# Performance work log

Hardware: AMD Instinct MI355X
Metric: run time of the kernel (lower is better)

Reference implementation:

```python
import jax, jax.numpy as jnp
import numpy as np

EPS = 1e-7  # K.epsilon()
ROUTINGS = 3

def squash(v):
    # v: [..., dim_capsule]
    s2 = jnp.sum(jnp.square(v), axis=-1, keepdims=True)
    scale = s2 / (1.0 + s2) / jnp.sqrt(s2 + EPS)
    return scale * v

def setup_inputs() -> dict:
    key = jax.random.key(0)
    k1, k2 = jax.random.split(key)
    B, IN_CAPS, IN_DIM = 256, 1152, 8
    NUM_CAPS, DIM_CAPS = 10, 16
    inputs = jax.random.normal(k1, (B, IN_CAPS, IN_DIM), dtype=jnp.float32)
    W = jax.random.normal(k2, (NUM_CAPS, IN_CAPS, DIM_CAPS, IN_DIM), dtype=jnp.float32) * 0.05
    return {"inputs": inputs, "W": W}

def reference(inputs, W):
    # inputs: [B, I, Q]; W: [J, I, P, Q]
    # inputs_hat[b,j,i,p] = sum_q W[j,i,p,q] * inputs[b,i,q]
    inputs_hat = jnp.einsum('jipq,biq->bjip', W, inputs)  # [B, J, I, P]
    B, J, I, P = inputs_hat.shape
    b = jnp.zeros((B, J, I), dtype=inputs_hat.dtype)
    outputs = None
    for r in range(ROUTINGS):
        c = jax.nn.softmax(b, axis=1)                      # over num_capsule J
        s = jnp.einsum('bji,bjip->bjp', c, inputs_hat)     # [B, J, P]
        outputs = squash(s)
        if r < ROUTINGS - 1:
            b = b + jnp.einsum('bjp,bjip->bji', outputs, inputs_hat)
    return outputs
```

## Files before the change

### kernel.cpp

```cpp
#include <hip/hip_runtime.h>

typedef _Float16 h2 __attribute__((ext_vector_type(2)));
typedef _Float16 h8 __attribute__((ext_vector_type(8)));
typedef float f4 __attribute__((ext_vector_type(4)));

#define BB 256
#define II 1152
#define QQ 8
#define JJ 10
#define PP 16

#define BT 16
#define IT 8
#define NBT (BB / BT)
#define NIT (II / IT)
#define XRH 72
#define WTILE (IT * PP * QQ)

#define NW (JJ * II * PP * QQ)
#define NX (BB * II * QQ)
#define NS (BB * JJ * PP)
#define LOG2E 1.4426950408889634f

template <int CTRL>
__device__ __forceinline__ float dpp_add(float v) {
    int s = __builtin_bit_cast(int, v);
    int t = __builtin_amdgcn_update_dpp(0, s, CTRL, 0xF, 0xF, true);
    return v + __builtin_bit_cast(float, t);
}
__device__ __forceinline__ float row_sum16(float v) {
    v = dpp_add<0xB1>(v);
    v = dpp_add<0x4E>(v);
    v = dpp_add<0x124>(v);
    v = dpp_add<0x128>(v);
    return v;
}
template <int CTRL>
__device__ __forceinline__ h2 dpp_add_pk(h2 v) {
    int s = __builtin_bit_cast(int, v);
    int t = __builtin_amdgcn_update_dpp(0, s, CTRL, 0xF, 0xF, true);
    return v + __builtin_bit_cast(h2, t);
}
__device__ __forceinline__ h2 row_sum16_pk(h2 v) {
    v = dpp_add_pk<0xB1>(v);
    v = dpp_add_pk<0x4E>(v);
    v = dpp_add_pk<0x124>(v);
    v = dpp_add_pk<0x128>(v);
    return v;
}

__device__ __forceinline__ float dot8(h8 w, h8 x) {
    h2 w0 = __builtin_shufflevector(w, w, 0, 1), w1 = __builtin_shufflevector(w, w, 2, 3);
    h2 w2 = __builtin_shufflevector(w, w, 4, 5), w3 = __builtin_shufflevector(w, w, 6, 7);
    h2 x0 = __builtin_shufflevector(x, x, 0, 1), x1 = __builtin_shufflevector(x, x, 2, 3);
    h2 x2 = __builtin_shufflevector(x, x, 4, 5), x3 = __builtin_shufflevector(x, x, 6, 7);
    float acc = __builtin_amdgcn_fdot2(w0, x0, 0.0f, false);
    acc = __builtin_amdgcn_fdot2(w1, x1, acc, false);
    acc = __builtin_amdgcn_fdot2(w2, x2, acc, false);
    acc = __builtin_amdgcn_fdot2(w3, x3, acc, false);
    return acc;
}

__global__ __launch_bounds__(256) void prep_kernel(
    const float* __restrict__ X, const float* __restrict__ W,
    _Float16* __restrict__ Xh, _Float16* __restrict__ Wh,
    float* __restrict__ S)
{
    const int g = blockIdx.x * 256 + threadIdx.x;
    const int stride = gridDim.x * 256;
    typedef _Float16 h4 __attribute__((ext_vector_type(4)));
    for (int k = g; k < NW / 4; k += stride) {
        const float4 f = ((const float4*)W)[k];
        h4 o = { (_Float16)f.x, (_Float16)f.y, (_Float16)f.z, (_Float16)f.w };
        ((h4*)Wh)[k] = o;
    }
    for (int k = g; k < NX / 4; k += stride) {
        const float4 f = ((const float4*)X)[k];
        h4 o = { (_Float16)f.x, (_Float16)f.y, (_Float16)f.z, (_Float16)f.w };
        ((h4*)Xh)[k] = o;
    }
    const float4 z = {0.f, 0.f, 0.f, 0.f};
    for (int k = g; k < 3 * NS / 4; k += stride) ((float4*)S)[k] = z;
}

__global__ __launch_bounds__(256) void s0_mfma_kernel(
    const _Float16* __restrict__ Xh, const _Float16* __restrict__ Wh,
    float* __restrict__ S0)
{
    const int wid  = blockIdx.x * 4 + (threadIdx.x >> 6);
    const int lane = threadIdx.x & 63;
    const int bt  = wid / 80;
    const int rem = wid % 80;
    const int j   = rem >> 3;
    const int kc  = rem & 7;
    const int b0  = bt * 16;
    const int m    = lane & 15;
    const int quad = lane >> 4;
    const int ib   = kc * 144;

    const _Float16* ax = Xh + ((size_t)(b0 + m) * II + ib + quad) * QQ;
    const _Float16* bw = Wh + (((size_t)j * II + ib + quad) * PP + m) * QQ;

    f4 acc = {0.f, 0.f, 0.f, 0.f};
    for (int t = 0; t < 36; ++t) {
        const h8 a = *(const h8*)ax;
        const h8 b = *(const h8*)bw;
        acc = __builtin_amdgcn_mfma_f32_16x16x32_f16(a, b, acc, 0, 0, 0);
        ax += 4 * QQ;
        bw += (size_t)4 * PP * QQ;
    }
#pragma unroll
    for (int r = 0; r < 4; ++r)
        atomicAdd(&S0[((size_t)(b0 + quad * 4 + r) * JJ + j) * PP + m], 0.1f * acc[r]);
}

template <int MODE>
__global__ __launch_bounds__(256) void vv_kernel(
    const float* __restrict__ S, float* __restrict__ V0raw,
    float* __restrict__ VV)
{
    const int idx = blockIdx.x * 256 + threadIdx.x;
    const float s = S[idx];
    const float n2 = row_sum16(s * s);
    const float sc = n2 * __builtin_amdgcn_rcpf(1.0f + n2)
                        * __builtin_amdgcn_rsqf(n2 + 1e-7f);
    const float v = s * sc;
    if (MODE == 0) {
        V0raw[idx] = v;
        VV[idx] = v * LOG2E;
    } else {
        VV[idx] = (v + V0raw[idx]) * LOG2E;
    }
}

__global__ __launch_bounds__(256, 4) void pass_kernel(
    const _Float16* __restrict__ Xh,
    const _Float16* __restrict__ Wh,
    const float* __restrict__ VV,
    float* __restrict__ Sout)
{
    __shared__ _Float16 ws[JJ * WTILE];
    __shared__ _Float16 xs[BT * XRH];

    const int bt = blockIdx.x & (NBT - 1);
    const int it = blockIdx.x >> 4;
    const int b0 = bt * BT;
    const int i0 = it * IT;
    const int tid = threadIdx.x;

    {
        const size_t jstride = (size_t)II * PP * QQ;
        const _Float16* wsrc = Wh + (size_t)i0 * PP * QQ;
#pragma unroll
        for (int k = 0; k < 5; ++k) {
            const int c = tid + k * 256;
            const int j = c >> 7;
            const int r = c & 127;
            *(h8*)(ws + j * WTILE + r * 8) = *(const h8*)(wsrc + j * jstride + r * 8);
        }
        if (tid < 128) {
            const int xb = tid >> 3;
            const int xr = tid & 7;
            *(h8*)(xs + xb * XRH + xr * 8) =
                *(const h8*)(Xh + ((size_t)(b0 + xb) * II + i0) * QQ + xr * 8);
        }
    }
    __syncthreads();

    const int b_l = tid >> 4;
    const int p   = tid & 15;
    const int b   = b0 + b_l;

    float vv[JJ];
#pragma unroll
    for (int j = 0; j < JJ; ++j)
        vv[j] = VV[((size_t)b * JJ + j) * PP + p];

    float sacc[JJ];
#pragma unroll
    for (int j = 0; j < JJ; ++j) sacc[j] = 0.0f;

    const _Float16* wb = ws + p * QQ;
    const _Float16* xb = xs + b_l * XRH;

#pragma unroll
    for (int i = 0; i < IT; ++i) {
        const h8 x8 = *(const h8*)(xb + i * QQ);

        float h[JJ];
#pragma unroll
        for (int j = 0; j < JJ; ++j)
            h[j] = dot8(*(const h8*)(wb + j * WTILE + i * PP * QQ), x8);

        float e[JJ];
#pragma unroll
        for (int jp = 0; jp < JJ; jp += 2) {
            const h2 pk = __builtin_bit_cast(h2,
                __builtin_amdgcn_cvt_pkrtz(vv[jp] * h[jp],
                                           vv[jp + 1] * h[jp + 1]));
            const h2 r = row_sum16_pk(pk);
            e[jp]     = __builtin_amdgcn_exp2f((float)r.x);
            e[jp + 1] = __builtin_amdgcn_exp2f((float)r.y);
        }
        float a0 = (e[0] + e[1]) + (e[2] + e[3]);
        float a1 = (e[4] + e[5]) + (e[6] + e[7]);
        const float sum = (a0 + a1) + (e[8] + e[9]);
        const float inv = __builtin_amdgcn_rcpf(sum);
#pragma unroll
        for (int j = 0; j < JJ; ++j) sacc[j] += (e[j] * inv) * h[j];
    }

#pragma unroll
    for (int j = 0; j < JJ; ++j)
        atomicAdd(&Sout[((size_t)b * JJ + j) * PP + p], sacc[j]);
}

__global__ __launch_bounds__(256) void squash_out_kernel(const float* __restrict__ S,
                                                         float* __restrict__ V)
{
    const int idx = blockIdx.x * blockDim.x + threadIdx.x;
    if (idx >= BB * JJ) return;
    const float4* sp = (const float4*)(S + idx * PP);
    float4 a = sp[0], b4 = sp[1], c4 = sp[2], d4 = sp[3];
    float s2 = a.x * a.x + a.y * a.y + a.z * a.z + a.w * a.w +
               b4.x * b4.x + b4.y * b4.y + b4.z * b4.z + b4.w * b4.w +
               c4.x * c4.x + c4.y * c4.y + c4.z * c4.z + c4.w * c4.w +
               d4.x * d4.x + d4.y * d4.y + d4.z * d4.z + d4.w * d4.w;
    const float scale = s2 / (1.0f + s2) / sqrtf(s2 + 1e-7f);
    a.x *= scale; a.y *= scale; a.z *= scale; a.w *= scale;
    b4.x *= scale; b4.y *= scale; b4.z *= scale; b4.w *= scale;
    c4.x *= scale; c4.y *= scale; c4.z *= scale; c4.w *= scale;
    d4.x *= scale; d4.y *= scale; d4.z *= scale; d4.w *= scale;
    float4* vp = (float4*)(V + idx * PP);
    vp[0] = a; vp[1] = b4; vp[2] = c4; vp[3] = d4;
}

extern "C" void kernel_launch(void* const* d_in, const int* in_sizes, int n_in,
                              void* d_out, int out_size, void* d_ws, size_t ws_size,
                              hipStream_t stream)
{
    const float* X = (const float*)d_in[0];
    const float* W = (const float*)d_in[1];
    float* out = (float*)d_out;

    _Float16* Xh = (_Float16*)d_ws;
    _Float16* Wh = Xh + NX;
    float* S0 = (float*)(Wh + NW);
    float* S1 = S0 + NS;
    float* S2 = S1 + NS;
    float* V0raw = S2 + NS;
    float* VV1   = V0raw + NS;
    float* VV2   = VV1 + NS;

    const int grid  = NBT * NIT;
    const int vgrid = NS / 256;

    prep_kernel<<<1024, 256, 0, stream>>>(X, W, Xh, Wh, S0);
    s0_mfma_kernel<<<320, 256, 0, stream>>>(Xh, Wh, S0);
    vv_kernel<0><<<vgrid, 256, 0, stream>>>(S0, V0raw, VV1);
    pass_kernel<<<grid, 256, 0, stream>>>(Xh, Wh, VV1, S1);
    vv_kernel<1><<<vgrid, 256, 0, stream>>>(S1, V0raw, VV2);
    pass_kernel<<<grid, 256, 0, stream>>>(Xh, Wh, VV2, S2);
    squash_out_kernel<<<10, 256, 0, stream>>>(S2, out);
}
```

Baseline: 132.0 us.

## Restructure routing pass kernel around MFMA for agreement and weighted sum

The routing pass drops per-thread fdot2 dot products and uses MFMA twice. One MFMA contracts v with W to get per-(b,i,q) projections, which are then scaled by x and reduced over q with DPP to form logits. A second MFMA multiplies c·x by W to accumulate s, with partial sums collected in shared memory before the global atomics. W is loaded into LDS in a transposed layout read via ds_read_b64_tr_b16, and VV is stored in fp16. This cuts VALU work in the hot kernel, at the cost of more LDS traffic, LDS atomics, a lower occupancy bound (3) and extra fp16 rounding.

```diff
diff --git a/kernel.cpp b/kernel.cpp
--- a/kernel.cpp
+++ b/kernel.cpp
@@ -1,6 +1,7 @@
 #include <hip/hip_runtime.h>
 
 typedef _Float16 h2 __attribute__((ext_vector_type(2)));
+typedef _Float16 h4 __attribute__((ext_vector_type(4)));
 typedef _Float16 h8 __attribute__((ext_vector_type(8)));
 typedef float f4 __attribute__((ext_vector_type(4)));
 
@@ -15,7 +16,6 @@
 #define NBT (BB / BT)
 #define NIT (II / IT)
 #define XRH 72
-#define WTILE (IT * PP * QQ)
 
 #define NW (JJ * II * PP * QQ)
 #define NX (BB * II * QQ)
@@ -41,24 +41,11 @@
     int t = __builtin_amdgcn_update_dpp(0, s, CTRL, 0xF, 0xF, true);
     return v + __builtin_bit_cast(h2, t);
 }
-__device__ __forceinline__ h2 row_sum16_pk(h2 v) {
+__device__ __forceinline__ h2 row_sum8_pk(h2 v) {
     v = dpp_add_pk<0xB1>(v);
     v = dpp_add_pk<0x4E>(v);
-    v = dpp_add_pk<0x124>(v);
-    v = dpp_add_pk<0x128>(v);
+    v = dpp_add_pk<0x141>(v);
     return v;
-}
-
-__device__ __forceinline__ float dot8(h8 w, h8 x) {
-    h2 w0 = __builtin_shufflevector(w, w, 0, 1), w1 = __builtin_shufflevector(w, w, 2, 3);
-    h2 w2 = __builtin_shufflevector(w, w, 4, 5), w3 = __builtin_shufflevector(w, w, 6, 7);
-    h2 x0 = __builtin_shufflevector(x, x, 0, 1), x1 = __builtin_shufflevector(x, x, 2, 3);
-    h2 x2 = __builtin_shufflevector(x, x, 4, 5), x3 = __builtin_shufflevector(x, x, 6, 7);
-    float acc = __builtin_amdgcn_fdot2(w0, x0, 0.0f, false);
-    acc = __builtin_amdgcn_fdot2(w1, x1, acc, false);
-    acc = __builtin_amdgcn_fdot2(w2, x2, acc, false);
-    acc = __builtin_amdgcn_fdot2(w3, x3, acc, false);
-    return acc;
 }
 
 __global__ __launch_bounds__(256) void prep_kernel(
@@ -68,7 +55,6 @@
 {
     const int g = blockIdx.x * 256 + threadIdx.x;
     const int stride = gridDim.x * 256;
-    typedef _Float16 h4 __attribute__((ext_vector_type(4)));
     for (int k = g; k < NW / 4; k += stride) {
         const float4 f = ((const float4*)W)[k];
         h4 o = { (_Float16)f.x, (_Float16)f.y, (_Float16)f.z, (_Float16)f.w };
@@ -117,7 +103,7 @@
 template <int MODE>
 __global__ __launch_bounds__(256) void vv_kernel(
     const float* __restrict__ S, float* __restrict__ V0raw,
-    float* __restrict__ VV)
+    _Float16* __restrict__ VVh)
 {
     const int idx = blockIdx.x * 256 + threadIdx.x;
     const float s = S[idx];
@@ -127,20 +113,25 @@
     const float v = s * sc;
     if (MODE == 0) {
         V0raw[idx] = v;
-        VV[idx] = v * LOG2E;
+        VVh[idx] = (_Float16)(v * LOG2E);
     } else {
-        VV[idx] = (v + V0raw[idx]) * LOG2E;
-    }
-}
-
-__global__ __launch_bounds__(256, 4) void pass_kernel(
+        VVh[idx] = (_Float16)((v + V0raw[idx]) * LOG2E);
+    }
+}
+
+__global__ __launch_bounds__(256, 3) void pass_kernel(
+    const float* __restrict__ X,
     const _Float16* __restrict__ Xh,
     const _Float16* __restrict__ Wh,
-    const float* __restrict__ VV,
+    const _Float16* __restrict__ VVh,
     float* __restrict__ Sout)
 {
-    __shared__ _Float16 ws[JJ * WTILE];
-    __shared__ _Float16 xs[BT * XRH];
+    __shared__ _Float16 wtr[JJ * 4 * 256];
+    __shared__ _Float16 xna[BT * XRH];
+    __shared__ float    xtr[64 * 20];
+    __shared__ _Float16 vvs[16 * 168];
+    __shared__ float    cs[4][JJ][2][16];
+    __shared__ float    sacc[JJ * 16 * 17];
 
     const int bt = blockIdx.x & (NBT - 1);
     const int it = blockIdx.x >> 4;
@@ -156,63 +147,131 @@
             const int c = tid + k * 256;
             const int j = c >> 7;
             const int r = c & 127;
-            *(h8*)(ws + j * WTILE + r * 8) = *(const h8*)(wsrc + j * jstride + r * 8);
+            const int i = r >> 4;
+            const int p = r & 15;
+            const h8 v = *(const h8*)(wsrc + j * jstride + (size_t)r * 8);
+            *(h8*)(wtr + (j * 4 + (i >> 1)) * 256 + p * 16 + (i & 1) * 8) = v;
         }
         if (tid < 128) {
             const int xb = tid >> 3;
             const int xr = tid & 7;
-            *(h8*)(xs + xb * XRH + xr * 8) =
+            *(h8*)(xna + xb * XRH + xr * 8) =
                 *(const h8*)(Xh + ((size_t)(b0 + xb) * II + i0) * QQ + xr * 8);
         }
+        {
+            const int qh = tid & 1;
+            const int i  = (tid >> 1) & 7;
+            const int b  = tid >> 4;
+            const float4 v = *(const float4*)(X + ((size_t)(b0 + b) * II + i0 + i) * QQ + qh * 4);
+            const int row = i * 8 + qh * 4;
+            xtr[(row + 0) * 20 + b] = v.x;
+            xtr[(row + 1) * 20 + b] = v.y;
+            xtr[(row + 2) * 20 + b] = v.z;
+            xtr[(row + 3) * 20 + b] = v.w;
+        }
+#pragma unroll
+        for (int k = 0; k < 5; ++k) {
+            const int c = tid + k * 256;
+            const int b = c / 80;
+            const int rem = c - b * 80;
+            *(unsigned*)(vvs + b * 168 + rem * 2) =
+                *(const unsigned*)(VVh + (size_t)(b0 + b) * JJ * PP + rem * 2);
+        }
+#pragma unroll
+        for (int k = 0; k < 3; ++k) {
+            const int c = tid + k * 256;
+            if (c < 680) ((f4*)sacc)[c] = f4{0.f, 0.f, 0.f, 0.f};
+        }
     }
     __syncthreads();
 
-    const int b_l = tid >> 4;
-    const int p   = tid & 15;
-    const int b   = b0 + b_l;
-
-    float vv[JJ];
+    const int lane = tid & 63;
+    const int wid  = tid >> 6;
+    const int nn   = lane & 15;
+    const int quad = lane >> 4;
+    const f4 zf4 = {0.f, 0.f, 0.f, 0.f};
+
+    h4 vvA[JJ];
 #pragma unroll
     for (int j = 0; j < JJ; ++j)
-        vv[j] = VV[((size_t)b * JJ + j) * PP + p];
-
-    float sacc[JJ];
-#pragma unroll
-    for (int j = 0; j < JJ; ++j) sacc[j] = 0.0f;
-
-    const _Float16* wb = ws + p * QQ;
-    const _Float16* xb = xs + b_l * XRH;
-
-#pragma unroll
-    for (int i = 0; i < IT; ++i) {
-        const h8 x8 = *(const h8*)(xb + i * QQ);
-
-        float h[JJ];
-#pragma unroll
-        for (int j = 0; j < JJ; ++j)
-            h[j] = dot8(*(const h8*)(wb + j * WTILE + i * PP * QQ), x8);
-
-        float e[JJ];
-#pragma unroll
-        for (int jp = 0; jp < JJ; jp += 2) {
-            const h2 pk = __builtin_bit_cast(h2,
-                __builtin_amdgcn_cvt_pkrtz(vv[jp] * h[jp],
-                                           vv[jp + 1] * h[jp + 1]));
-            const h2 r = row_sum16_pk(pk);
-            e[jp]     = __builtin_amdgcn_exp2f((float)r.x);
-            e[jp + 1] = __builtin_amdgcn_exp2f((float)r.y);
-        }
-        float a0 = (e[0] + e[1]) + (e[2] + e[3]);
-        float a1 = (e[4] + e[5]) + (e[6] + e[7]);
-        const float sum = (a0 + a1) + (e[8] + e[9]);
-        const float inv = __builtin_amdgcn_rcpf(sum);
-#pragma unroll
-        for (int j = 0; j < JJ; ++j) sacc[j] += (e[j] * inv) * h[j];
-    }
-
+        vvA[j] = *(const h4*)(vvs + nn * 168 + j * 16 + quad * 4);
+
+    const f4 xr = *(const f4*)(xtr + (wid * 16 + nn) * 20 + quad * 4);
+
+    const unsigned trbase =
+        (unsigned)(size_t)(const void*)wtr +
+        (unsigned)(wid * 512 + quad * 128 + nn * 8);
+
+    h4 bfrag[JJ];
+#pragma unroll
+    for (int j = 0; j < JJ; ++j) {
+        const unsigned a = trbase + (unsigned)(j * 2048);
+        asm volatile("ds_read_b64_tr_b16 %0, %1" : "=v"(bfrag[j]) : "v"(a));
+    }
+    asm volatile("s_waitcnt lgkmcnt(0)" ::: "memory");
+    __builtin_amdgcn_sched_barrier(0);
+
+    h2 lj0[JJ], lj1[JJ];
+#pragma unroll
+    for (int j = 0; j < JJ; ++j) {
+        const f4 U = __builtin_amdgcn_mfma_f32_16x16x16f16(vvA[j], bfrag[j], zf4, 0, 0, 0);
+        const h2 pk0 = __builtin_bit_cast(h2,
+            __builtin_amdgcn_cvt_pkrtz(U[0] * xr[0], U[1] * xr[1]));
+        const h2 pk1 = __builtin_bit_cast(h2,
+            __builtin_amdgcn_cvt_pkrtz(U[2] * xr[2], U[3] * xr[3]));
+        lj0[j] = row_sum8_pk(pk0);
+        lj1[j] = row_sum8_pk(pk1);
+    }
+
+    float e0[JJ], e1[JJ], e2[JJ], e3[JJ];
+#pragma unroll
+    for (int j = 0; j < JJ; ++j) {
+        e0[j] = __builtin_amdgcn_exp2f((float)lj0[j].x);
+        e1[j] = __builtin_amdgcn_exp2f((float)lj0[j].y);
+        e2[j] = __builtin_amdgcn_exp2f((float)lj1[j].x);
+        e3[j] = __builtin_amdgcn_exp2f((float)lj1[j].y);
+    }
+    float a0 = 0.f, a1 = 0.f, a2 = 0.f, a3 = 0.f;
+#pragma unroll
+    for (int j = 0; j < JJ; ++j) { a0 += e0[j]; a1 += e1[j]; a2 += e2[j]; a3 += e3[j]; }
+    const float v0 = __builtin_amdgcn_rcpf(a0);
+    const float v1 = __builtin_amdgcn_rcpf(a1);
+    const float v2 = __builtin_amdgcn_rcpf(a2);
+    const float v3 = __builtin_amdgcn_rcpf(a3);
+
+    if ((lane & 7) == 0) {
+        const int ii = nn >> 3;
+#pragma unroll
+        for (int j = 0; j < JJ; ++j) {
+            f4 c4v = { e0[j] * v0, e1[j] * v1, e2[j] * v2, e3[j] * v3 };
+            *(f4*)&cs[wid][j][ii][quad * 4] = c4v;
+        }
+    }
+
+    const h4 xf = *(const h4*)(xna + nn * XRH + (wid * 2 + (quad >> 1)) * 8 + (quad & 1) * 4);
+    const h2 xlo = __builtin_shufflevector(xf, xf, 0, 1);
+    const h2 xhi = __builtin_shufflevector(xf, xf, 2, 3);
+#pragma unroll
+    for (int j = 0; j < JJ; ++j) {
+        const float c = cs[wid][j][quad >> 1][nn];
+        const h2 cc = __builtin_bit_cast(h2, __builtin_amdgcn_cvt_pkrtz(c, c));
+        const h2 y0 = cc * xlo;
+        const h2 y1 = cc * xhi;
+        const h4 y = __builtin_shufflevector(y0, y1, 0, 1, 2, 3);
+        const h4 wf = *(const h4*)(wtr + (j * 4 + wid) * 256 + nn * 16 +
+                                   (quad >> 1) * 8 + (quad & 1) * 4);
+        const f4 C = __builtin_amdgcn_mfma_f32_16x16x16f16(y, wf, zf4, 0, 0, 0);
+#pragma unroll
+        for (int r = 0; r < 4; ++r)
+            atomicAdd(&sacc[(j * 16 + quad * 4 + r) * 17 + nn], C[r]);
+    }
+    __syncthreads();
+
+    const int bf = tid >> 4, pf = tid & 15;
 #pragma unroll
     for (int j = 0; j < JJ; ++j)
-        atomicAdd(&Sout[((size_t)b * JJ + j) * PP + p], sacc[j]);
+        atomicAdd(&Sout[((size_t)(b0 + bf) * JJ + j) * PP + pf],
+                  sacc[(j * 16 + bf) * 17 + pf]);
 }
 
 __global__ __launch_bounds__(256) void squash_out_kernel(const float* __restrict__ S,
@@ -249,17 +308,17 @@
     float* S1 = S0 + NS;
     float* S2 = S1 + NS;
     float* V0raw = S2 + NS;
-    float* VV1   = V0raw + NS;
-    float* VV2   = VV1 + NS;
+    _Float16* VVh1 = (_Float16*)(V0raw + NS);
+    _Float16* VVh2 = VVh1 + NS;
 
     const int grid  = NBT * NIT;
     const int vgrid = NS / 256;
 
     prep_kernel<<<1024, 256, 0, stream>>>(X, W, Xh, Wh, S0);
     s0_mfma_kernel<<<320, 256, 0, stream>>>(Xh, Wh, S0);
-    vv_kernel<0><<<vgrid, 256, 0, stream>>>(S0, V0raw, VV1);
-    pass_kernel<<<grid, 256, 0, stream>>>(Xh, Wh, VV1, S1);
-    vv_kernel<1><<<vgrid, 256, 0, stream>>>(S1, V0raw, VV2);
-    pass_kernel<<<grid, 256, 0, stream>>>(Xh, Wh, VV2, S2);
+    vv_kernel<0><<<vgrid, 256, 0, stream>>>(S0, V0raw, VVh1);
+    pass_kernel<<<grid, 256, 0, stream>>>(X, Xh, Wh, VVh1, S1);
+    vv_kernel<1><<<vgrid, 256, 0, stream>>>(S1, V0raw, VVh2);
+    pass_kernel<<<grid, 256, 0, stream>>>(X, Xh, Wh, VVh2, S2);
     squash_out_kernel<<<10, 256, 0, stream>>>(S2, out);
 }
```

New measurement: 340.8 us. 158% more time.

## Replace atomic accumulation in pass kernel with per-block partials and separate reduction

Applied to the files above, without the earlier changes.

Each pass block now writes its per-tile partial sums to a dedicated buffer instead of atomically adding into a shared S array. The following squash kernels (vvred and squash_out) reduce the 144 partials per output before squashing, and zero-initialisation of S1/S2 is dropped. This removes contended global atomics but adds a large partial buffer write and a strided reduction read per routing pass.

```diff
diff --git a/kernel.cpp b/kernel.cpp
--- a/kernel.cpp
+++ b/kernel.cpp
@@ -20,6 +20,7 @@
 #define NW (JJ * II * PP * QQ)
 #define NX (BB * II * QQ)
 #define NS (BB * JJ * PP)
+#define BLK2 (JJ * BT * PP)
 #define LOG2E 1.4426950408889634f
 
 template <int CTRL>
@@ -61,10 +62,28 @@
     return acc;
 }
 
+__device__ __forceinline__ float reduce_partials(const float* __restrict__ Part,
+                                                 int idx) {
+    const int b = idx / (JJ * PP);
+    const int r = idx - b * (JJ * PP);
+    const int bt  = b >> 4;
+    const int pos = (r >> 4) * 256 + (b & 15) * 16 + (r & 15);
+    const float* src = Part + (size_t)bt * BLK2 + pos;
+    float s0 = 0.f, s1 = 0.f, s2 = 0.f, s3 = 0.f;
+#pragma unroll 4
+    for (int it = 0; it < NIT; it += 4) {
+        s0 += src[(size_t)(it + 0) * (NBT * BLK2)];
+        s1 += src[(size_t)(it + 1) * (NBT * BLK2)];
+        s2 += src[(size_t)(it + 2) * (NBT * BLK2)];
+        s3 += src[(size_t)(it + 3) * (NBT * BLK2)];
+    }
+    return (s0 + s1) + (s2 + s3);
+}
+
 __global__ __launch_bounds__(256) void prep_kernel(
     const float* __restrict__ X, const float* __restrict__ W,
     _Float16* __restrict__ Xh, _Float16* __restrict__ Wh,
-    float* __restrict__ S)
+    float* __restrict__ S0)
 {
     const int g = blockIdx.x * 256 + threadIdx.x;
     const int stride = gridDim.x * 256;
@@ -80,7 +99,7 @@
         ((h4*)Xh)[k] = o;
     }
     const float4 z = {0.f, 0.f, 0.f, 0.f};
-    for (int k = g; k < 3 * NS / 4; k += stride) ((float4*)S)[k] = z;
+    for (int k = g; k < NS / 4; k += stride) ((float4*)S0)[k] = z;
 }
 
 __global__ __launch_bounds__(256) void s0_mfma_kernel(
@@ -114,8 +133,7 @@
         atomicAdd(&S0[((size_t)(b0 + quad * 4 + r) * JJ + j) * PP + m], 0.1f * acc[r]);
 }
 
-template <int MODE>
-__global__ __launch_bounds__(256) void vv_kernel(
+__global__ __launch_bounds__(256) void vv0_kernel(
     const float* __restrict__ S, float* __restrict__ V0raw,
     float* __restrict__ VV)
 {
@@ -125,19 +143,28 @@
     const float sc = n2 * __builtin_amdgcn_rcpf(1.0f + n2)
                         * __builtin_amdgcn_rsqf(n2 + 1e-7f);
     const float v = s * sc;
-    if (MODE == 0) {
-        V0raw[idx] = v;
-        VV[idx] = v * LOG2E;
-    } else {
-        VV[idx] = (v + V0raw[idx]) * LOG2E;
-    }
+    V0raw[idx] = v;
+    VV[idx] = v * LOG2E;
+}
+
+__global__ __launch_bounds__(256) void vvred_kernel(
+    const float* __restrict__ Part, const float* __restrict__ V0raw,
+    float* __restrict__ VV)
+{
+    const int idx = blockIdx.x * 256 + threadIdx.x;
+    const float s = reduce_partials(Part, idx);
+    const float n2 = row_sum16(s * s);
+    const float sc = n2 * __builtin_amdgcn_rcpf(1.0f + n2)
+                        * __builtin_amdgcn_rsqf(n2 + 1e-7f);
+    const float v = s * sc;
+    VV[idx] = (v + V0raw[idx]) * LOG2E;
 }
 
 __global__ __launch_bounds__(256, 4) void pass_kernel(
     const _Float16* __restrict__ Xh,
     const _Float16* __restrict__ Wh,
     const float* __restrict__ VV,
-    float* __restrict__ Sout)
+    float* __restrict__ Part)
 {
     __shared__ _Float16 ws[JJ * WTILE];
     __shared__ _Float16 xs[BT * XRH];
@@ -210,29 +237,20 @@
         for (int j = 0; j < JJ; ++j) sacc[j] += (e[j] * inv) * h[j];
     }
 
+    float* dst = Part + (size_t)blockIdx.x * BLK2;
 #pragma unroll
     for (int j = 0; j < JJ; ++j)
-        atomicAdd(&Sout[((size_t)b * JJ + j) * PP + p], sacc[j]);
-}
-
-__global__ __launch_bounds__(256) void squash_out_kernel(const float* __restrict__ S,
-                                                         float* __restrict__ V)
-{
-    const int idx = blockIdx.x * blockDim.x + threadIdx.x;
-    if (idx >= BB * JJ) return;
-    const float4* sp = (const float4*)(S + idx * PP);
-    float4 a = sp[0], b4 = sp[1], c4 = sp[2], d4 = sp[3];
-    float s2 = a.x * a.x + a.y * a.y + a.z * a.z + a.w * a.w +
-               b4.x * b4.x + b4.y * b4.y + b4.z * b4.z + b4.w * b4.w +
-               c4.x * c4.x + c4.y * c4.y + c4.z * c4.z + c4.w * c4.w +
-               d4.x * d4.x + d4.y * d4.y + d4.z * d4.z + d4.w * d4.w;
-    const float scale = s2 / (1.0f + s2) / sqrtf(s2 + 1e-7f);
-    a.x *= scale; a.y *= scale; a.z *= scale; a.w *= scale;
-    b4.x *= scale; b4.y *= scale; b4.z *= scale; b4.w *= scale;
-    c4.x *= scale; c4.y *= scale; c4.z *= scale; c4.w *= scale;
-    d4.x *= scale; d4.y *= scale; d4.z *= scale; d4.w *= scale;
-    float4* vp = (float4*)(V + idx * PP);
-    vp[0] = a; vp[1] = b4; vp[2] = c4; vp[3] = d4;
+        dst[j * 256 + tid] = sacc[j];
+}
+
+__global__ __launch_bounds__(256) void squash_out_kernel(
+    const float* __restrict__ Part, float* __restrict__ V)
+{
+    const int idx = blockIdx.x * 256 + threadIdx.x;
+    const float s = reduce_partials(Part, idx);
+    const float n2 = row_sum16(s * s);
+    const float scale = n2 / (1.0f + n2) / sqrtf(n2 + 1e-7f);
+    V[idx] = s * scale;
 }
 
 extern "C" void kernel_launch(void* const* d_in, const int* in_sizes, int n_in,
@@ -246,20 +264,19 @@
     _Float16* Xh = (_Float16*)d_ws;
     _Float16* Wh = Xh + NX;
     float* S0 = (float*)(Wh + NW);
-    float* S1 = S0 + NS;
-    float* S2 = S1 + NS;
-    float* V0raw = S2 + NS;
+    float* V0raw = S0 + NS;
     float* VV1   = V0raw + NS;
     float* VV2   = VV1 + NS;
+    float* Part  = VV2 + NS;
 
     const int grid  = NBT * NIT;
     const int vgrid = NS / 256;
 
     prep_kernel<<<1024, 256, 0, stream>>>(X, W, Xh, Wh, S0);
     s0_mfma_kernel<<<320, 256, 0, stream>>>(Xh, Wh, S0);
-    vv_kernel<0><<<vgrid, 256, 0, stream>>>(S0, V0raw, VV1);
-    pass_kernel<<<grid, 256, 0, stream>>>(Xh, Wh, VV1, S1);
-    vv_kernel<1><<<vgrid, 256, 0, stream>>>(S1, V0raw, VV2);
-    pass_kernel<<<grid, 256, 0, stream>>>(Xh, Wh, VV2, S2);
-    squash_out_kernel<<<10, 256, 0, stream>>>(S2, out);
-}
+    vv0_kernel<<<vgrid, 256, 0, stream>>>(S0, V0raw, VV1);
+    pass_kernel<<<grid, 256, 0, stream>>>(Xh, Wh, VV1, Part);
+    vvred_kernel<<<vgrid, 256, 0, stream>>>(Part, V0raw, VV2);
+    pass_kernel<<<grid, 256, 0, stream>>>(Xh, Wh, VV2, Part);
+    squash_out_kernel<<<vgrid, 256, 0, stream>>>(Part, out);
+}
```

After: 158.8 us. +20.3%, slower.

## Materialize fp16 prediction vectors once and reuse them in routing passes

Applied to the files above, without the earlier changes.

Replaces the MFMA s0 kernel with a kernel that computes all u_hat values, stores them packed as fp16 in workspace, and accumulates the first-iteration sum. The routing passes then read the precomputed u_hat instead of reloading W and X tiles and recomputing the dot products, and they use packed half multiplies for the agreement term. This removes the repeated dot-product compute but adds roughly 94MB of global writes plus reads per pass, and it lowers the precision of the s0 path relative to the MFMA version.

```diff
diff --git a/kernel.cpp b/kernel.cpp
--- a/kernel.cpp
+++ b/kernel.cpp
@@ -20,6 +20,7 @@
 #define NW (JJ * II * PP * QQ)
 #define NX (BB * II * QQ)
 #define NS (BB * JJ * PP)
+#define NH ((size_t)II * BB * 5 * 16)
 #define LOG2E 1.4426950408889634f
 
 template <int CTRL>
@@ -83,61 +84,11 @@
     for (int k = g; k < 3 * NS / 4; k += stride) ((float4*)S)[k] = z;
 }
 
-__global__ __launch_bounds__(256) void s0_mfma_kernel(
-    const _Float16* __restrict__ Xh, const _Float16* __restrict__ Wh,
-    float* __restrict__ S0)
-{
-    const int wid  = blockIdx.x * 4 + (threadIdx.x >> 6);
-    const int lane = threadIdx.x & 63;
-    const int bt  = wid / 80;
-    const int rem = wid % 80;
-    const int j   = rem >> 3;
-    const int kc  = rem & 7;
-    const int b0  = bt * 16;
-    const int m    = lane & 15;
-    const int quad = lane >> 4;
-    const int ib   = kc * 144;
-
-    const _Float16* ax = Xh + ((size_t)(b0 + m) * II + ib + quad) * QQ;
-    const _Float16* bw = Wh + (((size_t)j * II + ib + quad) * PP + m) * QQ;
-
-    f4 acc = {0.f, 0.f, 0.f, 0.f};
-    for (int t = 0; t < 36; ++t) {
-        const h8 a = *(const h8*)ax;
-        const h8 b = *(const h8*)bw;
-        acc = __builtin_amdgcn_mfma_f32_16x16x32_f16(a, b, acc, 0, 0, 0);
-        ax += 4 * QQ;
-        bw += (size_t)4 * PP * QQ;
-    }
-#pragma unroll
-    for (int r = 0; r < 4; ++r)
-        atomicAdd(&S0[((size_t)(b0 + quad * 4 + r) * JJ + j) * PP + m], 0.1f * acc[r]);
-}
-
-template <int MODE>
-__global__ __launch_bounds__(256) void vv_kernel(
-    const float* __restrict__ S, float* __restrict__ V0raw,
-    float* __restrict__ VV)
-{
-    const int idx = blockIdx.x * 256 + threadIdx.x;
-    const float s = S[idx];
-    const float n2 = row_sum16(s * s);
-    const float sc = n2 * __builtin_amdgcn_rcpf(1.0f + n2)
-                        * __builtin_amdgcn_rsqf(n2 + 1e-7f);
-    const float v = s * sc;
-    if (MODE == 0) {
-        V0raw[idx] = v;
-        VV[idx] = v * LOG2E;
-    } else {
-        VV[idx] = (v + V0raw[idx]) * LOG2E;
-    }
-}
-
-__global__ __launch_bounds__(256, 4) void pass_kernel(
+__global__ __launch_bounds__(256, 4) void hhat_s0_kernel(
     const _Float16* __restrict__ Xh,
     const _Float16* __restrict__ Wh,
-    const float* __restrict__ VV,
-    float* __restrict__ Sout)
+    unsigned* __restrict__ HH,
+    float* __restrict__ S0)
 {
     __shared__ _Float16 ws[JJ * WTILE];
     __shared__ _Float16 xs[BT * XRH];
@@ -171,17 +122,13 @@
     const int p   = tid & 15;
     const int b   = b0 + b_l;
 
-    float vv[JJ];
-#pragma unroll
-    for (int j = 0; j < JJ; ++j)
-        vv[j] = VV[((size_t)b * JJ + j) * PP + p];
-
     float sacc[JJ];
 #pragma unroll
     for (int j = 0; j < JJ; ++j) sacc[j] = 0.0f;
 
     const _Float16* wb = ws + p * QQ;
     const _Float16* xb = xs + b_l * XRH;
+    unsigned* hw = HH + ((size_t)i0 * BB + b) * 80 + p;
 
 #pragma unroll
     for (int i = 0; i < IT; ++i) {
@@ -192,13 +139,84 @@
         for (int j = 0; j < JJ; ++j)
             h[j] = dot8(*(const h8*)(wb + j * WTILE + i * PP * QQ), x8);
 
-        float e[JJ];
+#pragma unroll
+        for (int jp = 0; jp < JJ; jp += 2)
+            hw[(size_t)i * (BB * 80) + (jp >> 1) * 16] =
+                __builtin_bit_cast(unsigned,
+                    __builtin_amdgcn_cvt_pkrtz(h[jp], h[jp + 1]));
+
+#pragma unroll
+        for (int j = 0; j < JJ; ++j) sacc[j] += h[j];
+    }
+
+#pragma unroll
+    for (int j = 0; j < JJ; ++j)
+        atomicAdd(&S0[((size_t)b * JJ + j) * PP + p], 0.1f * sacc[j]);
+}
+
+template <int MODE>
+__global__ __launch_bounds__(256) void vv_kernel(
+    const float* __restrict__ S, float* __restrict__ V0raw,
+    float* __restrict__ VV)
+{
+    const int idx = blockIdx.x * 256 + threadIdx.x;
+    const float s = S[idx];
+    const float n2 = row_sum16(s * s);
+    const float sc = n2 * __builtin_amdgcn_rcpf(1.0f + n2)
+                        * __builtin_amdgcn_rsqf(n2 + 1e-7f);
+    const float v = s * sc;
+    if (MODE == 0) {
+        V0raw[idx] = v;
+        VV[idx] = v * LOG2E;
+    } else {
+        VV[idx] = (v + V0raw[idx]) * LOG2E;
+    }
+}
+
+__global__ __launch_bounds__(256, 6) void pass_kernel(
+    const unsigned* __restrict__ HH,
+    const float* __restrict__ VV,
+    float* __restrict__ Sout)
+{
+    const int bt = blockIdx.x & (NBT - 1);
+    const int it = blockIdx.x >> 4;
+    const int b0 = bt * BT;
+    const int i0 = it * IT;
+    const int tid = threadIdx.x;
+
+    const int b_l = tid >> 4;
+    const int p   = tid & 15;
+    const int b   = b0 + b_l;
+
+    h2 vvpk[5];
+#pragma unroll
+    for (int jp = 0; jp < JJ; jp += 2) {
+        vvpk[jp >> 1] = __builtin_bit_cast(h2, __builtin_amdgcn_cvt_pkrtz(
+            VV[((size_t)b * JJ + jp) * PP + p],
+            VV[((size_t)b * JJ + jp + 1) * PP + p]));
+    }
+
+    float sacc[JJ];
+#pragma unroll
+    for (int j = 0; j < JJ; ++j) sacc[j] = 0.0f;
+
+    const unsigned* hr = HH + ((size_t)i0 * BB + b) * 80 + p;
+
+#pragma unroll
+    for (int i = 0; i < IT; ++i) {
+        h2 hp[5];
+#pragma unroll
+        for (int jp5 = 0; jp5 < 5; ++jp5)
+            hp[jp5] = __builtin_bit_cast(h2,
+                hr[(size_t)i * (BB * 80) + jp5 * 16]);
+
+        float e[JJ], h[JJ];
 #pragma unroll
         for (int jp = 0; jp < JJ; jp += 2) {
-            const h2 pk = __builtin_bit_cast(h2,
-                __builtin_amdgcn_cvt_pkrtz(vv[jp] * h[jp],
-                                           vv[jp + 1] * h[jp + 1]));
-            const h2 r = row_sum16_pk(pk);
+            const h2 hpv = hp[jp >> 1];
+            h[jp]     = (float)hpv.x;
+            h[jp + 1] = (float)hpv.y;
+            const h2 r = row_sum16_pk(vvpk[jp >> 1] * hpv);
             e[jp]     = __builtin_amdgcn_exp2f((float)r.x);
             e[jp + 1] = __builtin_amdgcn_exp2f((float)r.y);
         }
@@ -251,15 +269,16 @@
     float* V0raw = S2 + NS;
     float* VV1   = V0raw + NS;
     float* VV2   = VV1 + NS;
+    unsigned* HH = (unsigned*)(VV2 + NS);
 
     const int grid  = NBT * NIT;
     const int vgrid = NS / 256;
 
     prep_kernel<<<1024, 256, 0, stream>>>(X, W, Xh, Wh, S0);
-    s0_mfma_kernel<<<320, 256, 0, stream>>>(Xh, Wh, S0);
+    hhat_s0_kernel<<<grid, 256, 0, stream>>>(Xh, Wh, HH, S0);
     vv_kernel<0><<<vgrid, 256, 0, stream>>>(S0, V0raw, VV1);
-    pass_kernel<<<grid, 256, 0, stream>>>(Xh, Wh, VV1, S1);
+    pass_kernel<<<grid, 256, 0, stream>>>(HH, VV1, S1);
     vv_kernel<1><<<vgrid, 256, 0, stream>>>(S1, V0raw, VV2);
-    pass_kernel<<<grid, 256, 0, stream>>>(Xh, Wh, VV2, S2);
+    pass_kernel<<<grid, 256, 0, stream>>>(HH, VV2, S2);
     squash_out_kernel<<<10, 256, 0, stream>>>(S2, out);
 }
```

New measurement: 146.1 us. 1.11x slower.
